# Performance work log

Measured on AMD Instinct MI355X. Metric: run time of the kernel, lower is better.

The kernel has to match this reference:

```python
import jax, jax.numpy as jnp
import numpy as np

B, D, A = 512, 32, 18          # batch, n_latent_dims (= n_heads), n_actions
FED, AED = 128, 64             # factor/action embed dims
VD = FED + AED                 # vdim = 192
KD = VD                        # kdim (key_embed_dim=None -> vdim)
HID = 256                      # per-head MLP hidden size
H = D                          # n_heads = n_latent_dims


def setup_inputs() -> dict:
    key = jax.random.key(0)
    ks = jax.random.split(key, 20)
    s = lambda i, shape: jax.random.normal(ks[i], shape, dtype=jnp.float32) * 0.05
    return {
        "features": jax.random.normal(ks[0], (B, D), dtype=jnp.float32),
        "actions": jax.random.uniform(ks[1], (B, A), dtype=jnp.float32),
        # linear projections (stored as [in, out], i.e. torch weight.T)
        "Wq": s(2, (A, KD)),  "bq": s(3, (KD,)),      # action_query_projection
        "Wk": s(4, (D, KD)),  "bk": s(5, (KD,)),      # factor_key_projection
        "Wav": s(6, (A, AED)), "bav": s(7, (AED,)),   # action_val_projection
        "Wfv": s(8, (D, FED)), "bfv": s(9, (FED,)),   # factor_val_projection
        # per-head input MLPs: vdim -> HID -> vdim (ReLU)
        "W1": s(10, (H, VD, HID)), "b1": s(11, (H, HID)),
        "W2": s(12, (H, HID, VD)), "b2": s(13, (H, VD)),
        # per-head output MLPs: vdim -> HID -> 1 (ReLU)
        "W1o": s(14, (H, VD, HID)), "b1o": s(15, (H, HID)),
        "W2o": s(16, (H, HID)),     "b2o": s(17, (H,)),
    }


def reference(features, actions, Wq, bq, Wk, bk, Wav, bav, Wfv, bfv,
              W1, b1, W2, b2, W1o, b1o, W2o, b2o):
    z, a = features, actions
    # diag_embed(z) row i = z_i * e_i, so Linear(diag_embed(z))[..., i, :] = z_i * W.T[i] + b.
    # z is expanded identically across heads, so factor embeds/keys are head-independent.
    factor_embeds = z[:, :, None] * Wfv[None] + bfv          # [B, D, FED]
    keys = z[:, :, None] * Wk[None] + bk                     # [B, D, KD]
    queries = a @ Wq + bq                                    # [B, KD]
    action_embeds = a @ Wav + bav                            # [B, AED]

    # concat factor vals with broadcast action vals -> [B, D, VD]
    cv = jnp.concatenate(
        [factor_embeds, jnp.broadcast_to(action_embeds[:, None, :], (B, D, AED))], axis=-1)

    # per-head input MLPs (ReLU), batched over heads via einsum
    h = jax.nn.relu(jnp.einsum('bdv,hvk->bhdk', cv, W1) + b1[None, :, None, :])
    values = jnp.einsum('bhdk,hkv->bhdv', h, W2) + b2[None, :, None, :]  # [B,H,D,VD]

    # attention: single query vs D keys; head-independent weights
    scores = (keys @ queries[:, :, None])[..., 0] / jnp.sqrt(jnp.float32(KD))  # [B, D]
    w = jax.nn.softmax(scores, axis=-1)                       # [B, D]
    attn_out = jnp.einsum('bd,bhdv->bhv', w, values)          # [B, H, VD]

    # per-head output MLPs (ReLU) -> scalar effect per head
    h2 = jax.nn.relu(jnp.einsum('bhv,hvk->bhk', attn_out, W1o) + b1o[None])
    effect = jnp.einsum('bhk,hk->bh', h2, W2o) + b2o[None]    # [B, H]

    attn_weights = jnp.broadcast_to(w[:, None, :], (B, H, D))  # [B, H, D]
    return effect, attn_weights
```

## Files before the change

kernel.cpp:

```cpp
#include <hip/hip_runtime.h>
#include <hip/hip_bf16.h>


typedef __attribute__((ext_vector_type(8))) short bf16x8;
typedef __attribute__((ext_vector_type(4))) short bf16x4;
typedef __attribute__((ext_vector_type(4))) float f32x4;

__device__ __forceinline__ short f2bf(float x) {
  unsigned u = __float_as_uint(x);
  u += 0x7fffu + ((u >> 16) & 1u);
  return (short)(u >> 16);
}

__global__ __launch_bounds__(256) void kA_prep(
    const float* __restrict__ feat, const float* __restrict__ act,
    const float* __restrict__ Wq, const float* __restrict__ bq,
    const float* __restrict__ Wk,
    const float* __restrict__ Wav, const float* __restrict__ bav,
    const float* __restrict__ Wfv, const float* __restrict__ bfv,
    const float* __restrict__ W1, const float* __restrict__ b1,
    const float* __restrict__ W2, const float* __restrict__ b2,
    const float* __restrict__ W1o, const float* __restrict__ b1o,
    float* __restrict__ ws_w, float* __restrict__ ws_ae,
    float* __restrict__ ws_U, float* __restrict__ ws_c0,
    unsigned short* __restrict__ ws_Mbf, float* __restrict__ ws_c1,
    float* __restrict__ out_aw) {
  __shared__ float sh[8448];
  const int bx = blockIdx.x;
  const int t = threadIdx.x;

  if (bx < 64) {
    const int b0 = bx * 8;
    float* sWk = sh;
    float* sA  = sh + 6144;
    float* sQk = sh + 6320;
    float* sW  = sh + 6944;
#pragma unroll
    for (int i = 0; i < 24; ++i) {
      const int idx = i * 256 + t;
      sWk[(idx % 192) * 32 + (idx / 192)] = Wk[idx];
    }
    if (t < 144) sA[t] = act[b0 * 18 + t];
    __syncthreads();
    for (int o = t; o < 608; o += 256) {
      const int j = o >> 5, d = o & 31;
      const float* arow = (j < 18) ? (Wq + j * 192) : bq;
      float acc = 0.f;
      for (int c = 0; c < 192; ++c) acc += arow[c] * sWk[c * 32 + d];
      sQk[o] = acc;
    }
    __syncthreads();
    {
      const int bi = t >> 5, d = t & 31;
      float dot = sQk[18 * 32 + d];
#pragma unroll
      for (int j = 0; j < 18; ++j) dot += sA[bi * 18 + j] * sQk[j * 32 + d];
      const float z = feat[b0 * 32 + t];
      float sc = z * dot * 0.07216878364870322f;
      float mx = sc;
#pragma unroll
      for (int off = 16; off >= 1; off >>= 1) mx = fmaxf(mx, __shfl_xor(mx, off, 64));
      const float e = __expf(sc - mx);
      float s = e;
#pragma unroll
      for (int off = 16; off >= 1; off >>= 1) s += __shfl_xor(s, off, 64);
      const float w = e / s;
      ws_w[b0 * 32 + t] = w;
      sW[t] = w;
    }
#pragma unroll
    for (int o = t; o < 512; o += 256) {
      const int bi = o >> 6, j = o & 63;
      float acc = bav[j];
#pragma unroll
      for (int jj = 0; jj < 18; ++jj) acc += sA[bi * 18 + jj] * Wav[jj * 64 + j];
      ws_ae[b0 * 64 + o] = acc;
    }
    __syncthreads();
#pragma unroll
    for (int i = 0; i < 32; ++i)
      out_aw[b0 * 1024 + i * 256 + t] = sW[(i >> 2) * 32 + (t & 31)];

  } else if (bx < 224) {
    const int r = bx - 64;
    const int h = r / 5, dt = r % 5;
    float* sF = sh;
    if (dt < 4) {
#pragma unroll
      for (int i = 0; i < 4; ++i) sF[i * 256 + t] = Wfv[dt * 1024 + i * 256 + t];
    } else {
      if (t < 128) sF[t] = bfv[t];
    }
    __syncthreads();
    if (dt < 4) {
      float acc[8];
#pragma unroll
      for (int dd = 0; dd < 8; ++dd) acc[dd] = 0.f;
      for (int fc = 0; fc < 32; ++fc) {
        float w1v[4];
#pragma unroll
        for (int u = 0; u < 4; ++u) w1v[u] = W1[(h * 192 + fc * 4 + u) * 256 + t];
#pragma unroll
        for (int dd = 0; dd < 8; ++dd) {
          float4 f4 = *(const float4*)(sF + dd * 128 + fc * 4);
          acc[dd] += f4.x * w1v[0] + f4.y * w1v[1] + f4.z * w1v[2] + f4.w * w1v[3];
        }
      }
#pragma unroll
      for (int dd = 0; dd < 8; ++dd)
        ws_U[(h * 32 + dt * 8 + dd) * 256 + t] = acc[dd];
    } else {
      float acc = b1[h * 256 + t];
      for (int fc = 0; fc < 32; ++fc) {
        float w1v[4];
#pragma unroll
        for (int u = 0; u < 4; ++u) w1v[u] = W1[(h * 192 + fc * 4 + u) * 256 + t];
        float4 f4 = *(const float4*)(sF + fc * 4);
        acc += f4.x * w1v[0] + f4.y * w1v[1] + f4.z * w1v[2] + f4.w * w1v[3];
      }
      ws_c0[h * 256 + t] = acc;
    }

  } else {
    const int r = bx - 224;
    const int h = r >> 4, kt = r & 15;
    float* s = sh;
#pragma unroll
    for (int i = 0; i < 12; ++i)
      s[i * 256 + t] = W2[h * 49152 + kt * 3072 + i * 256 + t];
    __syncthreads();
    float acc[16];
#pragma unroll
    for (int rr = 0; rr < 16; ++rr) acc[rr] = 0.f;
    float c1acc = 0.f;
    for (int vc = 0; vc < 48; ++vc) {
      float w1o[4], b2v[4];
#pragma unroll
      for (int u = 0; u < 4; ++u) {
        w1o[u] = W1o[(h * 192 + vc * 4 + u) * 256 + t];
        b2v[u] = b2[h * 192 + vc * 4 + u];
      }
      c1acc += b2v[0] * w1o[0] + b2v[1] * w1o[1] + b2v[2] * w1o[2] + b2v[3] * w1o[3];
#pragma unroll
      for (int rr = 0; rr < 16; ++rr) {
        float4 w2 = *(const float4*)(s + rr * 192 + vc * 4);
        acc[rr] += w2.x * w1o[0] + w2.y * w1o[1] + w2.z * w1o[2] + w2.w * w1o[3];
      }
    }
    if (kt == 0) ws_c1[h * 256 + t] = c1acc + b1o[h * 256 + t];
    __syncthreads();
#pragma unroll
    for (int rr = 0; rr < 16; ++rr) s[rr * 260 + t] = acc[rr];
    __syncthreads();
    const int k1l = t & 15, k2g = t >> 4;
#pragma unroll
    for (int it = 0; it < 16; ++it) {
      const int k2 = it * 16 + k2g;
      ws_Mbf[(h * 256 + k2) * 256 + kt * 16 + k1l] =
          (unsigned short)f2bf(s[k1l * 260 + k2]);
    }
  }
}

__global__ __launch_bounds__(256) void kB_main(
    const float* __restrict__ feat, const float* __restrict__ ws_w,
    const float* __restrict__ ws_U, const float* __restrict__ W1,
    const float* __restrict__ ws_ae, const float* __restrict__ ws_c0,
    const unsigned short* __restrict__ ws_Mbf, const float* __restrict__ ws_c1,
    const float* __restrict__ W2o, const float* __restrict__ b2o,
    float* __restrict__ out_eff) {
  const int bx = blockIdx.x;
  const int h = (bx & 7) * 4 + ((bx >> 3) & 3);
  const int bt = bx >> 5;
  const int b0 = bt * 16;
  const int t = threadIdx.x;

  __shared__ __align__(16) char smem[16896];
  short* sP   = (short*)smem;
  float* sAe  = (float*)(smem + 8448);
  float* sZ   = (float*)(smem + 12544);
  float* sWw  = (float*)(smem + 14592);
  float* sRed = (float*)(smem + 16640);

  {
#pragma unroll
    for (int i = 0; i < 2; ++i) {
      sZ[i * 256 + t]  = feat[b0 * 32 + i * 256 + t];
      sWw[i * 256 + t] = ws_w[b0 * 32 + i * 256 + t];
    }
#pragma unroll
    for (int i = 0; i < 4; ++i) sAe[i * 256 + t] = ws_ae[b0 * 64 + i * 256 + t];
  }
  __syncthreads();

  {
    const int bq = t >> 6, kg = t & 63;
    float g[4][4];

    {
      float4 c04 = *(const float4*)(ws_c0 + h * 256 + kg * 4);
#pragma unroll
      for (int r = 0; r < 4; ++r) {
        g[r][0] = c04.x; g[r][1] = c04.y; g[r][2] = c04.z; g[r][3] = c04.w;
      }
      const float* W1p = W1 + (h * 192 + 128) * 256 + kg * 4;
      for (int jc = 0; jc < 16; ++jc) {
        float w1q[4][4];
#pragma unroll
        for (int u = 0; u < 4; ++u) {
          float4 w4 = *(const float4*)(W1p + (jc * 4 + u) * 256);
          w1q[u][0] = w4.x; w1q[u][1] = w4.y; w1q[u][2] = w4.z; w1q[u][3] = w4.w;
        }
        float a4[4][4];
#pragma unroll
        for (int r = 0; r < 4; ++r) {
          float4 av = *(const float4*)(sAe + (bq * 4 + r) * 64 + jc * 4);
          a4[r][0] = av.x; a4[r][1] = av.y; a4[r][2] = av.z; a4[r][3] = av.w;
        }
#pragma unroll
        for (int u = 0; u < 4; ++u)
#pragma unroll
          for (int r = 0; r < 4; ++r)
#pragma unroll
            for (int c = 0; c < 4; ++c)
              g[r][c] += a4[r][u] * w1q[u][c];
      }
    }

    float acc[4][4];
#pragma unroll
    for (int r = 0; r < 4; ++r) {
      acc[r][0] = 0.f; acc[r][1] = 0.f; acc[r][2] = 0.f; acc[r][3] = 0.f;
    }
    const float* Up = ws_U + h * 8192 + kg * 4;
    for (int dc = 0; dc < 8; ++dc) {
      float uc[4][4];
#pragma unroll
      for (int dd = 0; dd < 4; ++dd) {
        float4 u4 = *(const float4*)(Up + (dc * 4 + dd) * 256);
        uc[dd][0] = u4.x; uc[dd][1] = u4.y; uc[dd][2] = u4.z; uc[dd][3] = u4.w;
      }
      float zr[4][4], wr[4][4];
#pragma unroll
      for (int r = 0; r < 4; ++r) {
        float4 z4 = *(const float4*)(sZ + (bq * 4 + r) * 32 + dc * 4);
        float4 w4 = *(const float4*)(sWw + (bq * 4 + r) * 32 + dc * 4);
        zr[r][0] = z4.x; zr[r][1] = z4.y; zr[r][2] = z4.z; zr[r][3] = z4.w;
        wr[r][0] = w4.x; wr[r][1] = w4.y; wr[r][2] = w4.z; wr[r][3] = w4.w;
      }
#pragma unroll
      for (int dd = 0; dd < 4; ++dd) {
#pragma unroll
        for (int r = 0; r < 4; ++r) {
#pragma unroll
          for (int c = 0; c < 4; ++c)
            acc[r][c] += wr[r][dd] * fmaxf(zr[r][dd] * uc[dd][c] + g[r][c], 0.f);
        }
      }
    }
#pragma unroll
    for (int r = 0; r < 4; ++r) {
      bf16x4 p;
#pragma unroll
      for (int c = 0; c < 4; ++c) p[c] = f2bf(acc[r][c]);
      *(bf16x4*)(sP + (bq * 4 + r) * 264 + kg * 4) = p;
    }
  }
  __syncthreads();

  {
    const int wv = t >> 6;
    const int lane = t & 63;
    const int quad = lane >> 4, l15 = lane & 15;

    f32x4 acc[4];
    const f32x4 zero = {0.f, 0.f, 0.f, 0.f};
#pragma unroll
    for (int nt = 0; nt < 4; ++nt) acc[nt] = zero;

    float c1r[4], w2r[4];
#pragma unroll
    for (int nt = 0; nt < 4; ++nt) {
      const int col = wv * 64 + nt * 16 + l15;
      c1r[nt] = ws_c1[h * 256 + col];
      w2r[nt] = W2o[h * 256 + col];
    }
    const unsigned short* Mp = ws_Mbf + (size_t)(h * 256 + wv * 64) * 256;

#pragma unroll
    for (int kc = 0; kc < 8; ++kc) {
      bf16x8 a0 = *(const bf16x8*)(sP + l15 * 264 + kc * 32 + quad * 8);
      bf16x8 bfr[4];
#pragma unroll
      for (int nt = 0; nt < 4; ++nt)
        bfr[nt] = *(const bf16x8*)(Mp + (nt * 16 + l15) * 256 + kc * 32 + quad * 8);
#pragma unroll
      for (int nt = 0; nt < 4; ++nt)
        acc[nt] = __builtin_amdgcn_mfma_f32_16x16x32_bf16(a0, bfr[nt], acc[nt], 0, 0, 0);
    }
#pragma unroll
    for (int r = 0; r < 4; ++r) {
      float s = fmaxf(acc[0][r] + c1r[0], 0.f) * w2r[0]
              + fmaxf(acc[1][r] + c1r[1], 0.f) * w2r[1]
              + fmaxf(acc[2][r] + c1r[2], 0.f) * w2r[2]
              + fmaxf(acc[3][r] + c1r[3], 0.f) * w2r[3];
      s += __shfl_xor(s, 1, 64);
      s += __shfl_xor(s, 2, 64);
      s += __shfl_xor(s, 4, 64);
      s += __shfl_xor(s, 8, 64);
      if (l15 == 0) sRed[(quad * 4 + r) * 4 + wv] = s;
    }
  }
  __syncthreads();
  if (t < 16) {
    float v = sRed[t * 4] + sRed[t * 4 + 1] + sRed[t * 4 + 2] + sRed[t * 4 + 3] + b2o[h];
    out_eff[(b0 + t) * 32 + h] = v;
  }
}

extern "C" void kernel_launch(void* const* d_in, const int* in_sizes, int n_in,
                              void* d_out, int out_size, void* d_ws, size_t ws_size,
                              hipStream_t stream) {
  const float* feat = (const float*)d_in[0];
  const float* act  = (const float*)d_in[1];
  const float* Wq   = (const float*)d_in[2];
  const float* bq   = (const float*)d_in[3];
  const float* Wk   = (const float*)d_in[4];
  const float* Wav  = (const float*)d_in[6];
  const float* bav  = (const float*)d_in[7];
  const float* Wfv  = (const float*)d_in[8];
  const float* bfv  = (const float*)d_in[9];
  const float* W1   = (const float*)d_in[10];
  const float* b1   = (const float*)d_in[11];
  const float* W2   = (const float*)d_in[12];
  const float* b2   = (const float*)d_in[13];
  const float* W1o  = (const float*)d_in[14];
  const float* b1o  = (const float*)d_in[15];
  const float* W2o  = (const float*)d_in[16];
  const float* b2o  = (const float*)d_in[17];
  float* out = (float*)d_out;
  float* ws = (float*)d_ws;

  float* ws_w  = ws;
  float* ws_ae = ws + 16384;
  float* ws_U  = ws + 49152;
  float* ws_c0 = ws + 311296;
  float* ws_c1 = ws + 319488;
  unsigned short* ws_Mbf = (unsigned short*)(ws + 327680);

  hipLaunchKernelGGL(kA_prep, dim3(736), dim3(256), 0, stream,
                     feat, act, Wq, bq, Wk, Wav, bav, Wfv, bfv, W1, b1,
                     W2, b2, W1o, b1o, ws_w, ws_ae, ws_U, ws_c0, ws_Mbf, ws_c1,
                     out + 16384);
  hipLaunchKernelGGL(kB_main, dim3(1024), dim3(256), 0, stream,
                     feat, ws_w, ws_U, W1, ws_ae, ws_c0, ws_Mbf, ws_c1,
                     W2o, b2o, out);
}
```

Before: 162.7 us.

## Register-tile W2·W1o fold in prep kernel with 4x4 outer products

```diff
diff --git a/kernel.cpp b/kernel.cpp
--- a/kernel.cpp
+++ b/kernel.cpp
@@ -125,39 +125,58 @@
     const int r = bx - 224;
     const int h = r >> 4, kt = r & 15;
     float* s = sh;
-#pragma unroll
-    for (int i = 0; i < 12; ++i)
-      s[i * 256 + t] = W2[h * 49152 + kt * 3072 + i * 256 + t];
-    __syncthreads();
-    float acc[16];
-#pragma unroll
-    for (int rr = 0; rr < 16; ++rr) acc[rr] = 0.f;
-    float c1acc = 0.f;
+    if (t < 192) {
+#pragma unroll
+      for (int rr = 0; rr < 16; ++rr)
+        s[rr * 200 + t] = W2[h * 49152 + kt * 3072 + rr * 192 + t];
+    }
+    __syncthreads();
+    const int k2q = t >> 2, rq = t & 3;
+    float acc[4][4];
+#pragma unroll
+    for (int r0 = 0; r0 < 4; ++r0)
+#pragma unroll
+      for (int c = 0; c < 4; ++c) acc[r0][c] = 0.f;
+    float c1acc[4] = {0.f, 0.f, 0.f, 0.f};
+    const float* W1op = W1o + h * 49152 + k2q * 4;
     for (int vc = 0; vc < 48; ++vc) {
-      float w1o[4], b2v[4];
+      float w1q[4][4];
 #pragma unroll
       for (int u = 0; u < 4; ++u) {
-        w1o[u] = W1o[(h * 192 + vc * 4 + u) * 256 + t];
-        b2v[u] = b2[h * 192 + vc * 4 + u];
-      }
-      c1acc += b2v[0] * w1o[0] + b2v[1] * w1o[1] + b2v[2] * w1o[2] + b2v[3] * w1o[3];
-#pragma unroll
-      for (int rr = 0; rr < 16; ++rr) {
-        float4 w2 = *(const float4*)(s + rr * 192 + vc * 4);
-        acc[rr] += w2.x * w1o[0] + w2.y * w1o[1] + w2.z * w1o[2] + w2.w * w1o[3];
-      }
-    }
-    if (kt == 0) ws_c1[h * 256 + t] = c1acc + b1o[h * 256 + t];
-    __syncthreads();
-#pragma unroll
-    for (int rr = 0; rr < 16; ++rr) s[rr * 260 + t] = acc[rr];
-    __syncthreads();
-    const int k1l = t & 15, k2g = t >> 4;
-#pragma unroll
-    for (int it = 0; it < 16; ++it) {
-      const int k2 = it * 16 + k2g;
-      ws_Mbf[(h * 256 + k2) * 256 + kt * 16 + k1l] =
-          (unsigned short)f2bf(s[k1l * 260 + k2]);
+        float4 w4 = *(const float4*)(W1op + (vc * 4 + u) * 256);
+        w1q[u][0] = w4.x; w1q[u][1] = w4.y; w1q[u][2] = w4.z; w1q[u][3] = w4.w;
+      }
+      float w2q[4][4];
+#pragma unroll
+      for (int r0 = 0; r0 < 4; ++r0) {
+        float4 w2 = *(const float4*)(s + (rq * 4 + r0) * 200 + vc * 4);
+        w2q[r0][0] = w2.x; w2q[r0][1] = w2.y; w2q[r0][2] = w2.z; w2q[r0][3] = w2.w;
+      }
+      float b2v[4];
+#pragma unroll
+      for (int u = 0; u < 4; ++u) b2v[u] = b2[h * 192 + vc * 4 + u];
+#pragma unroll
+      for (int u = 0; u < 4; ++u) {
+#pragma unroll
+        for (int c = 0; c < 4; ++c) c1acc[c] += b2v[u] * w1q[u][c];
+#pragma unroll
+        for (int r0 = 0; r0 < 4; ++r0)
+#pragma unroll
+          for (int c = 0; c < 4; ++c)
+            acc[r0][c] += w2q[r0][u] * w1q[u][c];
+      }
+    }
+#pragma unroll
+    for (int c = 0; c < 4; ++c) {
+      bf16x4 p;
+#pragma unroll
+      for (int r0 = 0; r0 < 4; ++r0) p[r0] = f2bf(acc[r0][c]);
+      *(bf16x4*)(ws_Mbf + (size_t)(h * 256 + k2q * 4 + c) * 256 + kt * 16 + rq * 4) = p;
+    }
+    if (kt == 0 && rq == 0) {
+#pragma unroll
+      for (int c = 0; c < 4; ++c)
+        ws_c1[h * 256 + k2q * 4 + c] = c1acc[c] + b1o[h * 256 + k2q * 4 + c];
     }
   }
 }
```

New measurement: 156.2 us. 4.0% less time.
